# Kernel optimization log

Hardware: AMD Instinct MI355X
Metric: run time of the kernel (lower is better)

## Reference

```python
import jax, jax.numpy as jnp
import numpy as np
from jax import lax

MAX_SIGMA = 20.0
TRUNCATE = 4.0  # scipy.ndimage.gaussian_filter default
R = int(TRUNCATE * MAX_SIGMA + 0.5)  # fixed max radius = 80 -> 161 taps


def setup_inputs() -> dict:
    key = jax.random.key(0)
    k1, k2 = jax.random.split(key)
    x = jax.random.normal(k1, (512, 256, 256), dtype=jnp.float32)
    blur_sigmas = jnp.geomspace(0.5, MAX_SIGMA, 32).astype(jnp.float32)
    fwd_steps = jax.random.randint(k2, (512,), 0, 32)
    return {"x": x, "blur_sigmas": blur_sigmas, "fwd_steps": fwd_steps}


def _per_sample_kernels(sigmas):
    # scipy gaussian_filter: radius_i = int(truncate*sigma + 0.5), kernel
    # phi(o) = exp(-o^2 / (2 sigma^2)) normalized over |o| <= radius_i.
    off = jnp.arange(-R, R + 1, dtype=jnp.float32)          # [2R+1]
    w = jnp.exp(-0.5 * (off[None, :] / sigmas[:, None]) ** 2)  # [B, 2R+1]
    rad = jnp.floor(TRUNCATE * sigmas + 0.5)[:, None]        # per-sample radius
    w = w * (jnp.abs(off)[None, :] <= rad)
    return w / jnp.sum(w, axis=-1, keepdims=True)


def _blur(x, kernels):
    # x: [B, H, W]; kernels: [B, 2R+1]. Separable depthwise conv, batch as
    # channels with feature_group_count=B; symmetric pad == scipy 'reflect'.
    B = x.shape[0]
    dn = ("NCHW", "OIHW", "NCHW")
    xp = jnp.pad(x, ((0, 0), (R, R), (R, R)), mode="symmetric")[None]  # [1,B,H+2R,W+2R]
    kh = kernels[:, None, :, None]  # [B,1,2R+1,1]
    kw = kernels[:, None, None, :]  # [B,1,1,2R+1]
    y = lax.conv_general_dilated(xp, kh, (1, 1), "VALID",
                                 dimension_numbers=dn, feature_group_count=B)
    y = lax.conv_general_dilated(y, kw, (1, 1), "VALID",
                                 dimension_numbers=dn, feature_group_count=B)
    return y[0]  # [B, H, W]


def reference(x, blur_sigmas, fwd_steps):
    sigmas = blur_sigmas[fwd_steps]           # [B] per-sample sigma
    kernels = _per_sample_kernels(sigmas)     # [B, 2R+1]
    return _blur(x, kernels)
```

## Files before the change

kernel.cpp:

```cpp
#include <hip/hip_runtime.h>

#define WDIM  256
#define NSAMP 512
#define NSIG  32
#define RB    64
#define NBAND 2048
#define QOFF  16
#define WOFF  65536

typedef float    f32x4 __attribute__((ext_vector_type(4)));
typedef _Float16 f16x8 __attribute__((ext_vector_type(8)));

__device__ __forceinline__ int reflect(int q) {
    q = (q < 0) ? (-q - 1) : q;
    return (q >= WDIM) ? (2 * WDIM - 1 - q) : q;
}

__global__ __launch_bounds__(256) void build_w(const float* __restrict__ sigmas,
                                               _Float16* __restrict__ Wg) {
    __shared__ float wl[161];
    __shared__ float red;
    int s = blockIdx.x, t = threadIdx.x;
    float sigma = sigmas[s];
    float radf = floorf(4.0f * sigma + 0.5f);
    if (t < 161) {
        float off = (float)(t - 80);
        float w = 0.0f;
        if (fabsf(off) <= radf) { float z = off / sigma; w = expf(-0.5f * z * z); }
        wl[t] = w;
    }
    __syncthreads();
    if (t < 64) {
        float v = wl[t] + wl[t + 64] + (t < 33 ? wl[t + 128] : 0.0f);
        #pragma unroll
        for (int o = 32; o > 0; o >>= 1) v += __shfl_down(v, o);
        if (t == 0) red = 1.0f / v;
    }
    __syncthreads();
    float rs = red;
    int i = t;
    _Float16* wrow = Wg + ((size_t)s << 16) + (i << 8);
    for (int rq = blockIdx.y * 4; rq < blockIdx.y * 4 + 4; ++rq) {
        f16x8 v;
        #pragma unroll
        for (int j = 0; j < 8; ++j) {
            int r = rq * 8 + j;
            int d1 = r - i, d2 = -r - 1 - i, d3 = 511 - r - i;
            float w = 0.0f;
            if (d1 >= -80 && d1 <= 80) w += wl[d1 + 80];
            if (d2 >= -80)             w += wl[d2 + 80];
            if (d3 <= 80)              w += wl[d3 + 80];
            v[j] = (_Float16)(w * rs);
        }
        *(f16x8*)(wrow + rq * 8) = v;
    }
}

__global__ void build_queue(const float* __restrict__ sigmas,
                            const int* __restrict__ steps,
                            int* __restrict__ q) {
    __shared__ int hist[32];
    __shared__ int base[32];
    int t = threadIdx.x;
    if (t < 32) hist[t] = 0;
    __syncthreads();
    int nb2[2];
    #pragma unroll
    for (int k = 0; k < 2; ++k) {
        int s = t + 256 * k;
        float sigma = sigmas[steps[s]];
        int rad = (int)floorf(4.0f * sigma + 0.5f);
        nb2[k] = (2 * rad + 15) >> 3;
        atomicAdd(&hist[nb2[k]], 1);
    }
    __syncthreads();
    if (t == 0) {
        int acc = 0;
        for (int bin = 31; bin >= 0; --bin) { base[bin] = acc; acc += hist[bin]; }
    }
    __syncthreads();
    #pragma unroll
    for (int k = 0; k < 2; ++k) {
        int s = t + 256 * k;
        int r = atomicAdd(&base[nb2[k]], 1);
        int x = r & 7;
        int p = r >> 3;
        #pragma unroll
        for (int jb = 0; jb < 4; ++jb)
            q[QOFF + (((p << 2) + jb) << 3) + x] = (s << 2) | jb;
    }
}

template <bool QUEUED>
__global__ __launch_bounds__(256, 4) void blur_mfma(const float* __restrict__ in,
                                                    float* __restrict__ out,
                                                    const float* __restrict__ sigmas,
                                                    const int* __restrict__ steps,
                                                    const int* __restrict__ q,
                                                    const _Float16* __restrict__ Wg) {
    __shared__ alignas(16) _Float16 YL[RB * WDIM];

    int e;
    if constexpr (QUEUED) e = q[QOFF + blockIdx.x];
    else { int bid = blockIdx.x; e = (bid & 7) * (NBAND / 8) + (bid >> 3); }
    int b  = e >> 2;
    int r0 = (e & 3) * RB;

    int s = steps[b];
    float sigma = sigmas[s];
    int rad = (int)floorf(4.0f * sigma + 0.5f);
    const _Float16* Wm = Wg + ((size_t)s << 16);
    const float*    Xb = in + ((size_t)b << 16);

    int ln = threadIdx.x & 63, wv = threadIdx.x >> 6;
    int lm = ln & 15, lq = ln >> 4;

    f32x4 acc[4][4];
    #pragma unroll
    for (int mt = 0; mt < 4; ++mt)
        #pragma unroll
        for (int nt = 0; nt < 4; ++nt) acc[mt][nt] = (f32x4)0.0f;

    int kt0 = max(0, r0 - rad) >> 5;
    int kt1 = min(WDIM - 1, r0 + RB - 1 + rad) >> 5;

    for (int kt = kt0; kt <= kt1; ++kt) {
        f16x8 af[4];
        #pragma unroll
        for (int mt = 0; mt < 4; ++mt)
            af[mt] = *(const f16x8*)(Wm + (size_t)(r0 + mt * 16 + lm) * WDIM + (kt << 5) + lq * 8);
        #pragma unroll
        for (int nt = 0; nt < 4; ++nt) {
            const float* xp = Xb + (size_t)((kt << 5) + lq * 8) * WDIM + wv * 64 + nt * 16 + lm;
            float xv[8];
            #pragma unroll
            for (int jj = 0; jj < 8; ++jj) xv[jj] = xp[jj * WDIM];
            f16x8 bf;
            #pragma unroll
            for (int jj = 0; jj < 8; ++jj) bf[jj] = (_Float16)xv[jj];
            #pragma unroll
            for (int mt = 0; mt < 4; ++mt)
                acc[mt][nt] = __builtin_amdgcn_mfma_f32_16x16x32_f16(af[mt], bf, acc[mt][nt], 0, 0, 0);
        }
    }

    #pragma unroll
    for (int mt = 0; mt < 4; ++mt)
        #pragma unroll
        for (int nt = 0; nt < 4; ++nt)
            #pragma unroll
            for (int g = 0; g < 4; ++g) {
                int i = mt * 16 + lq * 4 + g;
                int c = wv * 64 + nt * 16 + lm;
                YL[(i << 8) + (c ^ ((i & 7) << 3))] = (_Float16)acc[mt][nt][g];
            }
    __syncthreads();

    f32x4 hac[4][4];
    #pragma unroll
    for (int mt = 0; mt < 4; ++mt)
        #pragma unroll
        for (int nt = 0; nt < 4; ++nt) hac[mt][nt] = (f32x4)0.0f;

    int jlo = wv * 64;
    int hk0 = max(0, jlo - rad) >> 5;
    int hk1 = min(WDIM - 1, jlo + 63 + rad) >> 5;

    for (int kt = hk0; kt <= hk1; ++kt) {
        f16x8 af[4], bf[4];
        #pragma unroll
        for (int mt = 0; mt < 4; ++mt) {
            int i = mt * 16 + lm;
            int c0 = (kt << 5) + lq * 8;
            af[mt] = *(const f16x8*)&YL[(i << 8) + (c0 ^ ((i & 7) << 3))];
        }
        #pragma unroll
        for (int nt = 0; nt < 4; ++nt)
            bf[nt] = *(const f16x8*)(Wm + (size_t)(jlo + nt * 16 + lm) * WDIM + (kt << 5) + lq * 8);
        #pragma unroll
        for (int mt = 0; mt < 4; ++mt)
            #pragma unroll
            for (int nt = 0; nt < 4; ++nt)
                hac[mt][nt] = __builtin_amdgcn_mfma_f32_16x16x32_f16(af[mt], bf[nt], hac[mt][nt], 0, 0, 0);
    }

    float* ob = out + ((size_t)b << 16);
    #pragma unroll
    for (int mt = 0; mt < 4; ++mt)
        #pragma unroll
        for (int nt = 0; nt < 4; ++nt)
            #pragma unroll
            for (int g = 0; g < 4; ++g)
                ob[(size_t)(r0 + mt * 16 + lq * 4 + g) * WDIM + jlo + nt * 16 + lm] = hac[mt][nt][g];
}

__device__ __forceinline__ int make_weights161(int b, const float* __restrict__ sigmas,
                                               const int* __restrict__ steps,
                                               float* wl, float* red) {
    int t = threadIdx.x;
    float sigma = sigmas[steps[b]];
    float radf = floorf(4.0f * sigma + 0.5f);
    if (t < 192) {
        float w = 0.0f;
        if (t < 161) {
            float off = (float)(t - 80);
            if (fabsf(off) <= radf) { float z = off / sigma; w = expf(-0.5f * z * z); }
        }
        wl[t] = w;
    }
    __syncthreads();
    if (t < 64) {
        float v = wl[t] + wl[t + 64] + wl[t + 128];
        #pragma unroll
        for (int o = 32; o > 0; o >>= 1) v += __shfl_down(v, o);
        if (t == 0) red[0] = 1.0f / v;
    }
    __syncthreads();
    float rs = red[0];
    if (t < 161) wl[t] *= rs;
    __syncthreads();
    return (int)radf;
}

__global__ __launch_bounds__(256) void vblur_nt(const float* __restrict__ in,
                                                float* __restrict__ out,
                                                const float* __restrict__ sigmas,
                                                const int* __restrict__ steps) {
    __shared__ float wl[192];
    __shared__ float red[1];
    int bid = blockIdx.x;
    int b = bid >> 4, i0 = (bid & 15) * 16;
    int rad = make_weights161(b, sigmas, steps, wl, red);
    int j = threadIdx.x;
    const float* inb = in + (size_t)b * WDIM * WDIM;
    float acc[16];
    #pragma unroll
    for (int ii = 0; ii < 16; ++ii) acc[ii] = 0.0f;
    for (int u = -rad; u <= rad; ++u) {
        float w = wl[80 + u];
        #pragma unroll
        for (int ii = 0; ii < 16; ++ii)
            acc[ii] = fmaf(w, inb[reflect(i0 + ii + u) * WDIM + j], acc[ii]);
    }
    #pragma unroll
    for (int ii = 0; ii < 16; ++ii)
        out[((size_t)b * WDIM + (i0 + ii)) * WDIM + j] = acc[ii];
}

__global__ __launch_bounds__(256) void hblur_inplace(float* __restrict__ buf,
                                                     const float* __restrict__ sigmas,
                                                     const int* __restrict__ steps) {
    __shared__ float wl[192];
    __shared__ float red[1];
    __shared__ float rp[WDIM + 160];
    int bid = blockIdx.x;
    int b = bid >> 8, i = bid & 255;
    float* row = buf + ((size_t)b * WDIM + i) * WDIM;
    int t = threadIdx.x;
    for (int s = t; s < WDIM + 160; s += 256) rp[s] = row[reflect(s - 80)];
    int rad = make_weights161(b, sigmas, steps, wl, red);
    float acc = 0.0f;
    for (int u = -rad; u <= rad; ++u) acc = fmaf(wl[80 + u], rp[80 + t + u], acc);
    row[t] = acc;
}

extern "C" void kernel_launch(void* const* d_in, const int* in_sizes, int n_in,
                              void* d_out, int out_size, void* d_ws, size_t ws_size,
                              hipStream_t stream) {
    const float* x     = (const float*)d_in[0];
    const float* sig   = (const float*)d_in[1];
    const int*   steps = (const int*)d_in[2];
    float* out = (float*)d_out;

    const size_t need = (size_t)WOFF + (size_t)NSIG * WDIM * WDIM * 2;
    if (ws_size >= need) {
        int* q = (int*)d_ws;
        _Float16* Wg = (_Float16*)((char*)d_ws + WOFF);
        build_w<<<dim3(NSIG, 8), 256, 0, stream>>>(sig, Wg);
        build_queue<<<1, 256, 0, stream>>>(sig, steps, q);
        blur_mfma<true><<<NBAND, 256, 0, stream>>>(x, out, sig, steps, q, Wg);
    } else {
        vblur_nt<<<NSAMP * 16, 256, 0, stream>>>(x, out, sig, steps);
        hblur_inplace<<<NSAMP * WDIM, 256, 0, stream>>>(out, sig, steps);
    }
}
```

Before: 84.53 us.

## Software-pipeline global loads in both blur passes and pack metadata into queue

Double-buffers the input tile loads in the vertical pass and the weight loads in the horizontal pass so the next k-tile's global reads are issued before the current tile's MFMAs run. The horizontal pass's first weight load now goes out before the barrier. The work queue entries now also pack the sigma index and radius, so each block skips its dependent steps/sigmas lookups. Launch bounds drop from 4 to 2 waves-per-SIMD to make room for the extra prefetch registers, at the cost of occupancy.

```diff
diff --git a/kernel.cpp b/kernel.cpp
--- a/kernel.cpp
+++ b/kernel.cpp
@@ -64,12 +64,14 @@
     int t = threadIdx.x;
     if (t < 32) hist[t] = 0;
     __syncthreads();
-    int nb2[2];
+    int nb2[2], rd2[2], st2[2];
     #pragma unroll
     for (int k = 0; k < 2; ++k) {
-        int s = t + 256 * k;
-        float sigma = sigmas[steps[s]];
+        int samp = t + 256 * k;
+        int st = steps[samp];
+        float sigma = sigmas[st];
         int rad = (int)floorf(4.0f * sigma + 0.5f);
+        st2[k] = st; rd2[k] = rad;
         nb2[k] = (2 * rad + 15) >> 3;
         atomicAdd(&hist[nb2[k]], 1);
     }
@@ -81,18 +83,19 @@
     __syncthreads();
     #pragma unroll
     for (int k = 0; k < 2; ++k) {
-        int s = t + 256 * k;
+        int samp = t + 256 * k;
         int r = atomicAdd(&base[nb2[k]], 1);
         int x = r & 7;
         int p = r >> 3;
         #pragma unroll
         for (int jb = 0; jb < 4; ++jb)
-            q[QOFF + (((p << 2) + jb) << 3) + x] = (s << 2) | jb;
+            q[QOFF + (((p << 2) + jb) << 3) + x] =
+                samp | (jb << 9) | (st2[k] << 11) | (rd2[k] << 16);
     }
 }
 
 template <bool QUEUED>
-__global__ __launch_bounds__(256, 4) void blur_mfma(const float* __restrict__ in,
+__global__ __launch_bounds__(256, 2) void blur_mfma(const float* __restrict__ in,
                                                     float* __restrict__ out,
                                                     const float* __restrict__ sigmas,
                                                     const int* __restrict__ steps,
@@ -100,15 +103,20 @@
                                                     const _Float16* __restrict__ Wg) {
     __shared__ alignas(16) _Float16 YL[RB * WDIM];
 
-    int e;
-    if constexpr (QUEUED) e = q[QOFF + blockIdx.x];
-    else { int bid = blockIdx.x; e = (bid & 7) * (NBAND / 8) + (bid >> 3); }
-    int b  = e >> 2;
-    int r0 = (e & 3) * RB;
-
-    int s = steps[b];
-    float sigma = sigmas[s];
-    int rad = (int)floorf(4.0f * sigma + 0.5f);
+    int b, r0, s, rad;
+    if constexpr (QUEUED) {
+        int d = q[QOFF + blockIdx.x];
+        b   = d & 511;
+        r0  = ((d >> 9) & 3) << 6;
+        s   = (d >> 11) & 31;
+        rad = (d >> 16) & 127;
+    } else {
+        int bid = blockIdx.x;
+        int e = (bid & 7) * (NBAND / 8) + (bid >> 3);
+        b = e >> 2; r0 = (e & 3) * RB;
+        s = steps[b];
+        rad = (int)floorf(4.0f * sigmas[s] + 0.5f);
+    }
     const _Float16* Wm = Wg + ((size_t)s << 16);
     const float*    Xb = in + ((size_t)b << 16);
 
@@ -124,23 +132,41 @@
     int kt0 = max(0, r0 - rad) >> 5;
     int kt1 = min(WDIM - 1, r0 + RB - 1 + rad) >> 5;
 
-    for (int kt = kt0; kt <= kt1; ++kt) {
+    float xvc[4][8], xvn[4][8];
+
+    auto xload = [&](int kt, float (&dst)[4][8]) {
+        const float* xp = Xb + (size_t)((kt << 5) + lq * 8) * WDIM + wv * 64 + lm;
+        #pragma unroll
+        for (int nt = 0; nt < 4; ++nt)
+            #pragma unroll
+            for (int jj = 0; jj < 8; ++jj)
+                dst[nt][jj] = xp[(size_t)jj * WDIM + nt * 16];
+    };
+    auto vtile = [&](int kt, float (&xv)[4][8]) {
         f16x8 af[4];
         #pragma unroll
         for (int mt = 0; mt < 4; ++mt)
             af[mt] = *(const f16x8*)(Wm + (size_t)(r0 + mt * 16 + lm) * WDIM + (kt << 5) + lq * 8);
         #pragma unroll
         for (int nt = 0; nt < 4; ++nt) {
-            const float* xp = Xb + (size_t)((kt << 5) + lq * 8) * WDIM + wv * 64 + nt * 16 + lm;
-            float xv[8];
-            #pragma unroll
-            for (int jj = 0; jj < 8; ++jj) xv[jj] = xp[jj * WDIM];
             f16x8 bf;
             #pragma unroll
-            for (int jj = 0; jj < 8; ++jj) bf[jj] = (_Float16)xv[jj];
+            for (int jj = 0; jj < 8; ++jj) bf[jj] = (_Float16)xv[nt][jj];
             #pragma unroll
             for (int mt = 0; mt < 4; ++mt)
                 acc[mt][nt] = __builtin_amdgcn_mfma_f32_16x16x32_f16(af[mt], bf, acc[mt][nt], 0, 0, 0);
+        }
+    };
+
+    xload(kt0, xvc);
+    for (int kt = kt0; kt <= kt1; ++kt) {
+        if (kt < kt1) xload(kt + 1, xvn);
+        vtile(kt, xvc);
+        if (kt < kt1) {
+            #pragma unroll
+            for (int nt = 0; nt < 4; ++nt)
+                #pragma unroll
+                for (int jj = 0; jj < 8; ++jj) xvc[nt][jj] = xvn[nt][jj];
         }
     }
 
@@ -154,20 +180,29 @@
                 int c = wv * 64 + nt * 16 + lm;
                 YL[(i << 8) + (c ^ ((i & 7) << 3))] = (_Float16)acc[mt][nt][g];
             }
-    __syncthreads();
-
-    f32x4 hac[4][4];
-    #pragma unroll
-    for (int mt = 0; mt < 4; ++mt)
-        #pragma unroll
-        for (int nt = 0; nt < 4; ++nt) hac[mt][nt] = (f32x4)0.0f;
 
     int jlo = wv * 64;
     int hk0 = max(0, jlo - rad) >> 5;
     int hk1 = min(WDIM - 1, jlo + 63 + rad) >> 5;
 
+    f16x8 bfc[4], bfn[4];
+    auto wload = [&](int kt, f16x8 (&bf)[4]) {
+        #pragma unroll
+        for (int nt = 0; nt < 4; ++nt)
+            bf[nt] = *(const f16x8*)(Wm + (size_t)(jlo + nt * 16 + lm) * WDIM + (kt << 5) + lq * 8);
+    };
+    wload(hk0, bfc);
+    __syncthreads();
+
+    f32x4 hac[4][4];
+    #pragma unroll
+    for (int mt = 0; mt < 4; ++mt)
+        #pragma unroll
+        for (int nt = 0; nt < 4; ++nt) hac[mt][nt] = (f32x4)0.0f;
+
     for (int kt = hk0; kt <= hk1; ++kt) {
-        f16x8 af[4], bf[4];
+        if (kt < hk1) wload(kt + 1, bfn);
+        f16x8 af[4];
         #pragma unroll
         for (int mt = 0; mt < 4; ++mt) {
             int i = mt * 16 + lm;
@@ -175,13 +210,14 @@
             af[mt] = *(const f16x8*)&YL[(i << 8) + (c0 ^ ((i & 7) << 3))];
         }
         #pragma unroll
-        for (int nt = 0; nt < 4; ++nt)
-            bf[nt] = *(const f16x8*)(Wm + (size_t)(jlo + nt * 16 + lm) * WDIM + (kt << 5) + lq * 8);
-        #pragma unroll
         for (int mt = 0; mt < 4; ++mt)
             #pragma unroll
             for (int nt = 0; nt < 4; ++nt)
-                hac[mt][nt] = __builtin_amdgcn_mfma_f32_16x16x32_f16(af[mt], bf[nt], hac[mt][nt], 0, 0, 0);
+                hac[mt][nt] = __builtin_amdgcn_mfma_f32_16x16x32_f16(af[mt], bfc[nt], hac[mt][nt], 0, 0, 0);
+        if (kt < hk1) {
+            #pragma unroll
+            for (int nt = 0; nt < 4; ++nt) bfc[nt] = bfn[nt];
+        }
     }
 
     float* ob = out + ((size_t)b << 16);
```

New measurement: 84.90 us (median of 2 runs). Within noise of the previous version (+0.4%).
